# Optimization experiments

Measured on AMD Instinct MI355X. Metric: run time of the kernel, lower is better.

## Reference

```python
import jax, jax.numpy as jnp
import numpy as np

NUM_NODES = 100
WINDOW = 128
GH = 256       # graph_hidden_channels
DH = 64        # discrepancy_hidden_channels
OUT = 128      # out_channels
B = 256        # graphs per batch
N = B * NUM_NODES
E = 409600


def _mconv(x, w, b):
    # x: [B, n, W], w: [n, 2, k], b: [n, 2]  (per-node Conv1d(1,2,k), 'same' padding)
    k = w.shape[-1]
    W = x.shape[-1]
    p = k // 2
    xp = jnp.pad(x, ((0, 0), (0, 0), (p, p)))
    win = jnp.stack([xp[..., j:j + W] for j in range(k)], axis=-1)  # [B,n,W,k]
    return jnp.einsum('bnwk,nck->bncw', win, w) + b[None, :, :, None]


def _gcn(x, edge_index, Wg, bg):
    # PyG GCNConv: add self-loops, symmetric normalization, then linear
    Nn = x.shape[0]
    xw = x @ Wg.T
    loops = jnp.arange(Nn, dtype=edge_index.dtype)
    src = jnp.concatenate([edge_index[0], loops])
    dst = jnp.concatenate([edge_index[1], loops])
    deg = jax.ops.segment_sum(jnp.ones(src.shape[0], dtype=xw.dtype), dst, num_segments=Nn)
    norm = jax.lax.rsqrt(jnp.maximum(deg, 1e-12))
    coef = norm[src] * norm[dst]
    agg = jax.ops.segment_sum(coef[:, None] * xw[src], dst, num_segments=Nn)
    return agg + bg


def setup_inputs() -> dict:
    key = jax.random.key(0)
    ks = jax.random.split(key, 20)
    f = 6 * WINDOW
    s = lambda d: 1.0 / np.sqrt(d)
    inp = {
        'x1': jax.random.normal(ks[0], (N, WINDOW), jnp.float32),
        'x2': jax.random.normal(ks[1], (N, WINDOW), jnp.float32),
        'edge_index1': jax.random.randint(ks[2], (2, E), 0, N, jnp.int32),
        'edge_index2': jax.random.randint(ks[3], (2, E), 0, N, jnp.int32),
        'w3': jax.random.normal(ks[4], (NUM_NODES, 2, 3), jnp.float32) * s(3),
        'b3': jax.random.normal(ks[5], (NUM_NODES, 2), jnp.float32) * s(3),
        'w5': jax.random.normal(ks[6], (NUM_NODES, 2, 5), jnp.float32) * s(5),
        'b5': jax.random.normal(ks[7], (NUM_NODES, 2), jnp.float32) * s(5),
        'w7': jax.random.normal(ks[8], (NUM_NODES, 2, 7), jnp.float32) * s(7),
        'b7': jax.random.normal(ks[9], (NUM_NODES, 2), jnp.float32) * s(7),
        'Wff': jax.random.normal(ks[10], (NUM_NODES, GH, f), jnp.float32) * s(f),
        'bff': jax.random.normal(ks[11], (NUM_NODES, GH), jnp.float32) * s(f),
        'Wg': jax.random.normal(ks[12], (GH, GH), jnp.float32) * s(GH),
        'bg': jax.random.normal(ks[13], (GH,), jnp.float32) * s(GH),
        'Wd': jax.random.normal(ks[14], (NUM_NODES, DH, 2 * GH), jnp.float32) * s(2 * GH),
        'bd': jax.random.normal(ks[15], (NUM_NODES, DH), jnp.float32) * s(2 * GH),
        'Wfc': jax.random.normal(ks[16], (OUT, NUM_NODES * DH), jnp.float32) * s(NUM_NODES * DH),
        'bfc': jax.random.normal(ks[17], (OUT,), jnp.float32) * s(NUM_NODES * DH),
    }
    return inp


def reference(x1, x2, edge_index1, edge_index2, w3, b3, w5, b5, w7, b7,
              Wff, bff, Wg, bg, Wd, bd, Wfc, bfc):
    n = w3.shape[0]
    Nn, W = x1.shape
    Bg = Nn // n

    def branch(x):
        xg = x.reshape(Bg, n, W)
        # multiscale CNN: concat conv3/conv5/conv7 along channel -> [B,n,6,W]
        c = jnp.concatenate([_mconv(xg, w3, b3), _mconv(xg, w5, b5), _mconv(xg, w7, b7)], axis=2)
        c = jax.nn.relu(c.reshape(Bg, n, 6 * W))            # channel-major flatten (matches view(-1))
        h = jax.nn.relu(jnp.einsum('bnf,nhf->bnh', c, Wff) + bff)
        return h.reshape(Nn, -1)

    h1 = jax.nn.relu(_gcn(branch(x1), edge_index1, Wg, bg))
    h2 = jax.nn.relu(_gcn(branch(x2), edge_index2, Wg, bg))
    H = h1.shape[-1]
    cat = jnp.concatenate([h1.reshape(Bg, n, H), h2.reshape(Bg, n, H)], axis=-1)  # [B,n,2H]
    d = jnp.einsum('bnf,ndf->bnd', cat, Wd) + bd            # per-node discrepancy FC
    du = jax.nn.relu(d.reshape(Bg, -1))                     # node-major -> [B, n*DH]
    return du @ Wfc.T + bfc
```

## Files before the change

kernel.cpp:

```cpp
#include <hip/hip_runtime.h>

#define DI __device__ __forceinline__

typedef __bf16 bf16_t;
typedef bf16_t bf16x8 __attribute__((ext_vector_type(8)));
typedef float f32x4 __attribute__((ext_vector_type(4)));
typedef ushort ushort8v __attribute__((ext_vector_type(8)));

static constexpr int NNODE = 100, WIN = 128, GH = 256, DH = 64, OUTC = 128, NB = 256;
static constexpr int NTOT = NB * NNODE;
static constexpr int NE = 409600;
static constexpr int FFK = 6 * WIN;
static constexpr size_t CB = (size_t)NNODE * NB * FFK;
static constexpr size_t HB = (size_t)NTOT * GH;
static constexpr int CVT_BLKS = 23264;
static constexpr int NSEG = 64, SEGE = NE / NSEG;
static constexpr int NPK = NTOT / 2;

DI ushort f2bf(float f) {
  union { float f; unsigned u; } v; v.f = f;
  unsigned r = v.u + 0x7fffu + ((v.u >> 16) & 1u);
  return (ushort)(r >> 16);
}
DI float bf2f(ushort s) {
  union { unsigned u; float f; } v; v.u = ((unsigned)s) << 16; return v.f;
}
DI float u2f(uint u) { union { uint u; float f; } v; v.u = u; return v.f; }

DI void gload16(const void* g, void* l) {
  __builtin_amdgcn_global_load_lds((const __attribute__((address_space(1))) void*)g,
                                   (__attribute__((address_space(3))) void*)l, 16, 0, 0);
}


DI void cvt_body(int bx, const float* s0, const float* s1, const float* s2, const float* s3,
                 ushort* d0, ushort* d1, ushort* d2, ushort* d3) {
  int j = bx * 256 + threadIdx.x;
  const float* s; ushort* d;
  if (j < 19660800 / 4) { s = s0; d = d0; }
  else if ((j -= 19660800 / 4) < 3276800 / 4) { s = s1; d = d1; }
  else if ((j -= 3276800 / 4) < 819200 / 4) { s = s2; d = d2; }
  else { j -= 819200 / 4; s = s3; d = d3; }
  float4 v = reinterpret_cast<const float4*>(s)[j];
  ushort4 o;
  o.x = f2bf(v.x); o.y = f2bf(v.y); o.z = f2bf(v.z); o.w = f2bf(v.w);
  reinterpret_cast<ushort4*>(d)[j] = o;
}

DI void histseg_body(int bx, const int* e1d, const int* e2d,
                     ushort* rank_local, uint* segcnt, uint* cnt ) {
  int set = bx & 1, seg = bx >> 1;
  int tid = threadIdx.x;
#pragma unroll
  for (int k = 0; k < NPK / 256; ++k) cnt[tid + k * 256] = 0;
  __syncthreads();
  const int* dstp = (set ? e2d : e1d) + seg * SEGE;
  ushort* rl = rank_local + set * NE + seg * SEGE;
#pragma unroll
  for (int k = 0; k < SEGE / 256; ++k) {
    int i = k * 256 + tid;
    int d = dstp[i];
    uint sh = (d & 1) * 16;
    uint old = atomicAdd(&cnt[d >> 1], 1u << sh);
    rl[i] = (ushort)((old >> sh) & 0xffffu);
  }
  __syncthreads();
  uint* sc = segcnt + (size_t)(set * NSEG + seg) * NPK;
#pragma unroll
  for (int k = 0; k < NPK / 256; ++k) sc[tid + k * 256] = cnt[tid + k * 256];
}

DI void fill_body(int bx, const int* e1, const int* e2, const int* offs,
                  const ushort* rank_local, const uint* segbase, int* csr) {
  int i = bx * 256 + threadIdx.x;
  int set = i >= NE;
  int ii = i - set * NE;
  const int* e = set ? e2 : e1;
  int d = e[NE + ii];
  int seg = ii / SEGE;
  uint b32 = segbase[(size_t)(set * NSEG + seg) * NPK + (d >> 1)];
  int base = (b32 >> ((d & 1) * 16)) & 0xffff;
  int pos = offs[set * (NTOT + 1) + d] + base + rank_local[i];
  csr[set * NE + pos] = e[ii];
}

DI void scan_body(int set, const int* deg_, int* offs_, float* norm_) {
  const int* deg = deg_ + set * NTOT;
  int* offs = offs_ + set * (NTOT + 1);
  float* norm = norm_ + set * NTOT;
  __shared__ int part[256];
  int t = threadIdx.x;
  int base = t * 100;
  int s = 0;
  for (int j = 0; j < 100; ++j) s += deg[base + j];
  part[t] = s;
  __syncthreads();
  for (int d = 1; d < 256; d <<= 1) {
    int vv = (t >= d) ? part[t - d] : 0;
    __syncthreads();
    part[t] += vv;
    __syncthreads();
  }
  int run = (t > 0) ? part[t - 1] : 0;
  for (int j = 0; j < 100; ++j) {
    int dv = deg[base + j];
    offs[base + j] = run;
    norm[base + j] = rsqrtf((float)(dv + 1));
    run += dv;
  }
  if (t == 255) offs[NTOT] = part[255];
}

DI void conv_body(int bx, const float* x1, const float* x2,
                  const float* w3, const float* b3, const float* w5, const float* b5,
                  const float* w7, const float* b7, ushort* c, float* xs ) {
  const int t = threadIdx.x;
  const int rowi = t >> 4;
  const int idx = t & 15;
  int r = bx * 16 + rowi;
  int br = r >= NTOT;
  int rr = r - br * NTOT;
  const float* x = br ? x2 : x1;
  int b = rr / 100, node = rr - b * 100;

  float* row = xs + rowi * 136;
  const int w0 = idx * 8;
  float4 v0 = *reinterpret_cast<const float4*>(x + (size_t)rr * WIN + w0);
  float4 v1 = *reinterpret_cast<const float4*>(x + (size_t)rr * WIN + w0 + 4);
  *reinterpret_cast<float4*>(&row[4 + w0]) = v0;
  *reinterpret_cast<float4*>(&row[4 + w0 + 4]) = v1;
  if (idx == 0) { row[0] = 0.f; row[1] = 0.f; row[2] = 0.f; row[3] = 0.f; }
  if (idx == 15) { row[132] = 0.f; row[133] = 0.f; row[134] = 0.f; row[135] = 0.f; }
  __syncthreads();

  float xv[14];
#pragma unroll
  for (int j = 0; j < 14; ++j) xv[j] = row[1 + w0 + j];

  const float* W3 = w3 + node * 6;  const float* B3 = b3 + node * 2;
  const float* W5 = w5 + node * 10; const float* B5 = b5 + node * 2;
  const float* W7 = w7 + node * 14; const float* B7 = b7 + node * 2;
  ushort* out = c + (size_t)br * CB + (size_t)(node * NB + b) * FFK + w0;

#pragma unroll
  for (int ch = 0; ch < 2; ++ch) {
    float k3[3], k5[5], k7[7];
#pragma unroll
    for (int j = 0; j < 3; ++j) k3[j] = W3[ch * 3 + j];
#pragma unroll
    for (int j = 0; j < 5; ++j) k5[j] = W5[ch * 5 + j];
#pragma unroll
    for (int j = 0; j < 7; ++j) k7[j] = W7[ch * 7 + j];
    float bb3 = B3[ch], bb5 = B5[ch], bb7 = B7[ch];
    ushort8v o3, o5, o7;
#pragma unroll
    for (int p = 0; p < 8; ++p) {
      float a3 = bb3, a5 = bb5, a7 = bb7;
#pragma unroll
      for (int j = 0; j < 3; ++j) a3 += k3[j] * xv[p + 2 + j];
#pragma unroll
      for (int j = 0; j < 5; ++j) a5 += k5[j] * xv[p + 1 + j];
#pragma unroll
      for (int j = 0; j < 7; ++j) a7 += k7[j] * xv[p + j];
      o3[p] = f2bf(fmaxf(a3, 0.f));
      o5[p] = f2bf(fmaxf(a5, 0.f));
      o7[p] = f2bf(fmaxf(a7, 0.f));
    }
    *reinterpret_cast<ushort8v*>(out + (0 + ch) * WIN) = o3;
    *reinterpret_cast<ushort8v*>(out + (2 + ch) * WIN) = o5;
    *reinterpret_cast<ushort8v*>(out + (4 + ch) * WIN) = o7;
  }
}

template <int MODE>
DI void gemm_body(int bx, int by, const ushort* __restrict__ A, const ushort* __restrict__ A2,
                  const ushort* __restrict__ Bm, ushort* __restrict__ obf,
                  float* __restrict__ of, const float* __restrict__ bias) {
  constexpr int BN = (MODE == 2) ? 64 : 128;
  constexpr int KT = (MODE == 0) ? 12 : (MODE == 1) ? 4 : (MODE == 2) ? 8 : 4;
  constexpr int LDA = (MODE == 0) ? 768 : (MODE == 1) ? 256 : (MODE == 2) ? 256 : 6400;
  constexpr int LDB = (MODE == 0) ? 768 : (MODE == 1) ? 256 : (MODE == 2) ? 512 : 6400;
  constexpr int MF = (MODE == 2) ? 2 : 4;
  constexpr int NF = 4;

  __shared__ ushort As[128 * 64];
  __shared__ ushort Bs[BN * 64];

  const int tid = threadIdx.x, wv = tid >> 6, lane = tid & 63;
  const int j8 = (((lane & 7) ^ (lane >> 3)) - (lane & 7)) * 8;

  int mt = 0, nt = 0, node = 0, kbase = 0, br = 0;
  if constexpr (MODE == 0) {
    int h = bx;
    int s = (h & 7) * 100 + (h >> 3);
    nt = s & 1; int rest = s >> 1;
    mt = rest & 1; int yy = rest >> 1;
    br = yy >= 100; node = yy - br * 100;
  } else if constexpr (MODE == 1) {
    int h = bx;
    int s = (h & 7) * 100 + (h >> 3);
    nt = s & 1; int rest = s >> 1;
    br = rest >= 200; mt = rest - br * 200;
  } else if constexpr (MODE == 2) { mt = bx; node = by; }
  else { mt = bx; kbase = by * 256; }

  const ushort* Ab = nullptr; const ushort* Bb = nullptr;
  if constexpr (MODE == 0) { Ab = A + (size_t)br * CB + (size_t)node * (NB * FFK) + (size_t)mt * 128 * FFK;
                             Bb = Bm + (size_t)node * (GH * FFK) + (size_t)nt * 128 * FFK; }
  else if constexpr (MODE == 1) { Ab = A + (size_t)br * HB + (size_t)mt * 128 * GH;
                                  Bb = Bm + (size_t)nt * 128 * GH; }
  else if constexpr (MODE == 2) { Bb = Bm + (size_t)node * (DH * 512); }
  else { Ab = A + (size_t)mt * 128 * 6400 + kbase; Bb = Bm + kbase; }

  const int wr = (MODE == 2) ? wv : (wv >> 1);
  const int wc = (MODE == 2) ? 0 : (wv & 1);

  f32x4 acc[MF][NF] = {};

  for (int kt = 0; kt < KT; ++kt) {
    const int k0 = kt * 64;
    __syncthreads();
#pragma unroll
    for (int it = 0; it < 4; ++it) {
      int rb = it * 32 + wv * 8;
      int row = rb + (lane >> 3);
      const ushort* gp;
      if constexpr (MODE == 2) {
        int b_ = mt * 128 + row;
        const ushort* src = (k0 < 256) ? A : A2;
        gp = src + (size_t)(b_ * NNODE + node) * GH + (k0 & 255) + (lane & 7) * 8 + j8;
      } else {
        gp = Ab + (size_t)row * LDA + k0 + (lane & 7) * 8 + j8;
      }
      gload16(gp, &As[rb * 64]);
    }
#pragma unroll
    for (int it = 0; it < BN / 32; ++it) {
      int rb = it * 32 + wv * 8;
      int row = rb + (lane >> 3);
      gload16(Bb + (size_t)row * LDB + k0 + (lane & 7) * 8 + j8, &Bs[rb * 64]);
    }
    __syncthreads();
#pragma unroll
    for (int kk = 0; kk < 2; ++kk) {
      const int ch8 = ((kk * 4 + (lane >> 4)) ^ (lane & 7)) * 8;
      bf16x8 af[MF], bfr[NF];
#pragma unroll
      for (int m = 0; m < MF; ++m) {
        int rr = wr * (MF * 16) + m * 16 + (lane & 15);
        af[m] = *reinterpret_cast<const bf16x8*>(&As[rr * 64 + ch8]);
      }
#pragma unroll
      for (int n = 0; n < NF; ++n) {
        int rr = wc * 64 + n * 16 + (lane & 15);
        bfr[n] = *reinterpret_cast<const bf16x8*>(&Bs[rr * 64 + ch8]);
      }
#pragma unroll
      for (int m = 0; m < MF; ++m)
#pragma unroll
        for (int n = 0; n < NF; ++n)
          acc[m][n] = __builtin_amdgcn_mfma_f32_16x16x32_bf16(af[m], bfr[n], acc[m][n], 0, 0, 0);
    }
  }

  const int lrow = (lane >> 4) * 4, lcol = lane & 15;
#pragma unroll
  for (int m = 0; m < MF; ++m) {
#pragma unroll
    for (int n = 0; n < NF; ++n) {
      int cc = wc * 64 + n * 16 + lcol;
#pragma unroll
      for (int rg = 0; rg < 4; ++rg) {
        int rr = wr * (MF * 16) + m * 16 + lrow + rg;
        float val = acc[m][n][rg];
        if constexpr (MODE == 0) {
          int b_ = mt * 128 + rr;
          int col = nt * 128 + cc;
          val = fmaxf(val + bias[node * GH + col], 0.f);
          obf[(size_t)br * HB + (size_t)(b_ * NNODE + node) * GH + col] = f2bf(val);
        } else if constexpr (MODE == 1) {
          int R = mt * 128 + rr;
          int col = nt * 128 + cc;
          obf[(size_t)br * HB + (size_t)R * GH + col] = f2bf(val * bias[br * NTOT + R]);
        } else if constexpr (MODE == 2) {
          int b_ = mt * 128 + rr;
          val = fmaxf(val + bias[node * DH + cc], 0.f);
          obf[(size_t)b_ * (NNODE * DH) + node * DH + cc] = f2bf(val);
        } else {
          int R = mt * 128 + rr;
          if (by == 0) val += bias[cc];
          atomicAdd(&of[R * OUTC + cc], val);
        }
      }
    }
  }
}


__global__ __launch_bounds__(256) void fused1_k(
    const float* __restrict__ Wff, const float* __restrict__ Wd,
    const float* __restrict__ Wfc, const float* __restrict__ Wg,
    ushort* __restrict__ Wffb, ushort* __restrict__ Wdb,
    ushort* __restrict__ Wfcb, ushort* __restrict__ Wgb,
    const int* __restrict__ e1d, const int* __restrict__ e2d,
    ushort* __restrict__ rank_local, uint* __restrict__ segcnt,
    const float* __restrict__ x1, const float* __restrict__ x2,
    const float* __restrict__ w3, const float* __restrict__ b3,
    const float* __restrict__ w5, const float* __restrict__ b5,
    const float* __restrict__ w7, const float* __restrict__ b7,
    ushort* __restrict__ c) {
  __shared__ uint smem[NPK];
  int bx = blockIdx.x;
  if (bx < 128) histseg_body(bx, e1d, e2d, rank_local, segcnt, smem);
  else if (bx < 3328) conv_body(bx - 128, x1, x2, w3, b3, w5, b5, w7, b7, c, (float*)smem);
  else cvt_body(bx - 3328, Wff, Wd, Wfc, Wg, Wffb, Wdb, Wfcb, Wgb);
}

__global__ __launch_bounds__(256) void segscan_k(const uint* __restrict__ segcnt,
                                                 uint* __restrict__ segbase, int* __restrict__ deg) {
  int set = blockIdx.y;
  int p = blockIdx.x * 256 + threadIdx.x;
  uint lo = 0, hi = 0;
  const uint* sc = segcnt + (size_t)set * NSEG * NPK + p;
  uint* sb = segbase + (size_t)set * NSEG * NPK + p;
  for (int s = 0; s < NSEG; ++s) {
    uint v = sc[(size_t)s * NPK];
    sb[(size_t)s * NPK] = lo | (hi << 16);
    lo += v & 0xffffu; hi += v >> 16;
  }
  reinterpret_cast<int2*>(deg)[set * NPK + p] = make_int2((int)lo, (int)hi);
}

__global__ __launch_bounds__(256) void scan_k(const int* __restrict__ deg,
                                              int* __restrict__ offs, float* __restrict__ nrm) {
  scan_body(blockIdx.x, deg, offs, nrm);
}

__global__ __launch_bounds__(256) void fused3_k(
    const ushort* __restrict__ cbuf, const ushort* __restrict__ Wffb,
    ushort* __restrict__ h, const float* __restrict__ bff,
    const int* __restrict__ e1, const int* __restrict__ e2,
    const int* __restrict__ offs, const ushort* __restrict__ rank_local,
    const uint* __restrict__ segbase, int* __restrict__ csr) {
  if ((int)blockIdx.x < 800)
    gemm_body<0>(blockIdx.x, 0, cbuf, nullptr, Wffb, h, nullptr, bff);
  else
    fill_body(blockIdx.x - 800, e1, e2, offs, rank_local, segbase, csr);
}

template <int MODE>
__global__ __launch_bounds__(256) void gemm_k(const ushort* __restrict__ A, const ushort* __restrict__ A2,
                                              const ushort* __restrict__ Bm, ushort* __restrict__ obf,
                                              float* __restrict__ of, const float* __restrict__ bias) {
  gemm_body<MODE>(blockIdx.x, blockIdx.y, A, A2, Bm, obf, of, bias);
}

__global__ __launch_bounds__(256) void agg_k(const ushort* __restrict__ xw_, const int* __restrict__ offs_,
                                             const int* __restrict__ csr_, const float* __restrict__ norm_,
                                             const float* __restrict__ bg, ushort* __restrict__ hg_) {
  int bid = blockIdx.x;
  int c = bid & 7;
  int i = bid >> 3;
  int br = c >> 2, slice = c & 3;
  int g = threadIdx.x >> 3;
  int v = i * 32 + g;
  int l8 = threadIdx.x & 7;
  int col = slice * 64 + l8 * 8;

  const ushort* xw = xw_ + (size_t)br * HB;
  const int* offs = offs_ + br * (NTOT + 1);
  const int* csr = csr_ + br * NE;
  const float* norm = norm_ + br * NTOT;
  ushort* hg = hg_ + (size_t)br * HB;
  const uint* base = reinterpret_cast<const uint*>(xw + col);

  float a[8];
  {
    uint4 q = *reinterpret_cast<const uint4*>(base + (size_t)v * (GH / 2));
    a[0] = u2f(q.x << 16); a[1] = u2f(q.x & 0xffff0000u);
    a[2] = u2f(q.y << 16); a[3] = u2f(q.y & 0xffff0000u);
    a[4] = u2f(q.z << 16); a[5] = u2f(q.z & 0xffff0000u);
    a[6] = u2f(q.w << 16); a[7] = u2f(q.w & 0xffff0000u);
  }
  int e0 = offs[v], e1v = offs[v + 1];
  int j = e0;
  for (; j + 1 < e1v; j += 2) {
    int s0 = csr[j], s1 = csr[j + 1];
    uint4 q0 = *reinterpret_cast<const uint4*>(base + (size_t)s0 * (GH / 2));
    uint4 q1 = *reinterpret_cast<const uint4*>(base + (size_t)s1 * (GH / 2));
    a[0] += u2f(q0.x << 16) + u2f(q1.x << 16);
    a[1] += u2f(q0.x & 0xffff0000u) + u2f(q1.x & 0xffff0000u);
    a[2] += u2f(q0.y << 16) + u2f(q1.y << 16);
    a[3] += u2f(q0.y & 0xffff0000u) + u2f(q1.y & 0xffff0000u);
    a[4] += u2f(q0.z << 16) + u2f(q1.z << 16);
    a[5] += u2f(q0.z & 0xffff0000u) + u2f(q1.z & 0xffff0000u);
    a[6] += u2f(q0.w << 16) + u2f(q1.w << 16);
    a[7] += u2f(q0.w & 0xffff0000u) + u2f(q1.w & 0xffff0000u);
  }
  if (j < e1v) {
    int s0 = csr[j];
    uint4 q0 = *reinterpret_cast<const uint4*>(base + (size_t)s0 * (GH / 2));
    a[0] += u2f(q0.x << 16); a[1] += u2f(q0.x & 0xffff0000u);
    a[2] += u2f(q0.y << 16); a[3] += u2f(q0.y & 0xffff0000u);
    a[4] += u2f(q0.z << 16); a[5] += u2f(q0.z & 0xffff0000u);
    a[6] += u2f(q0.w << 16); a[7] += u2f(q0.w & 0xffff0000u);
  }

  float nv = norm[v];
  float4 bb0 = *reinterpret_cast<const float4*>(bg + col);
  float4 bb1 = *reinterpret_cast<const float4*>(bg + col + 4);
  ushort8v o;
  o[0] = f2bf(fmaxf(nv * a[0] + bb0.x, 0.f));
  o[1] = f2bf(fmaxf(nv * a[1] + bb0.y, 0.f));
  o[2] = f2bf(fmaxf(nv * a[2] + bb0.z, 0.f));
  o[3] = f2bf(fmaxf(nv * a[3] + bb0.w, 0.f));
  o[4] = f2bf(fmaxf(nv * a[4] + bb1.x, 0.f));
  o[5] = f2bf(fmaxf(nv * a[5] + bb1.y, 0.f));
  o[6] = f2bf(fmaxf(nv * a[6] + bb1.z, 0.f));
  o[7] = f2bf(fmaxf(nv * a[7] + bb1.w, 0.f));
  *reinterpret_cast<ushort8v*>(hg + (size_t)v * GH + col) = o;
}

extern "C" void kernel_launch(void* const* d_in, const int* in_sizes, int n_in,
                              void* d_out, int out_size, void* d_ws, size_t ws_size,
                              hipStream_t stream) {
  const float* x1 = (const float*)d_in[0];
  const float* x2 = (const float*)d_in[1];
  const int* e1 = (const int*)d_in[2];
  const int* e2 = (const int*)d_in[3];
  const float* w3 = (const float*)d_in[4];  const float* b3 = (const float*)d_in[5];
  const float* w5 = (const float*)d_in[6];  const float* b5 = (const float*)d_in[7];
  const float* w7 = (const float*)d_in[8];  const float* b7 = (const float*)d_in[9];
  const float* Wff = (const float*)d_in[10]; const float* bff = (const float*)d_in[11];
  const float* Wg = (const float*)d_in[12];  const float* bg = (const float*)d_in[13];
  const float* Wd = (const float*)d_in[14];  const float* bd = (const float*)d_in[15];
  const float* Wfc = (const float*)d_in[16]; const float* bfc = (const float*)d_in[17];
  float* out = (float*)d_out;

  char* ws = (char*)d_ws;
  size_t off = 0;
  auto alloc = [&](size_t bytes) -> char* {
    char* p = ws + off;
    off = (off + bytes + 255) & ~(size_t)255;
    return p;
  };
  ushort* Wffb = (ushort*)alloc(19660800ull * 2);
  ushort* Wdb  = (ushort*)alloc(3276800ull * 2);
  ushort* Wfcb = (ushort*)alloc(819200ull * 2);
  ushort* Wgb  = (ushort*)alloc(65536ull * 2);
  ushort* cbuf = (ushort*)alloc(2 * CB * 2);
  ushort* h    = (ushort*)alloc(2 * HB * 2);
  ushort* xw   = (ushort*)alloc(2 * HB * 2);
  int* deg     = (int*)alloc(2 * NTOT * 4);
  int* offs    = (int*)alloc(2 * (NTOT + 1) * 4);
  ushort* rankl = (ushort*)alloc(2 * NE * 2);
  uint* segcnt  = (uint*)alloc((size_t)2 * NSEG * NPK * 4);
  uint* segbase = (uint*)alloc((size_t)2 * NSEG * NPK * 4);
  int* csr     = (int*)alloc(2 * NE * 4);
  float* nrm   = (float*)alloc(2 * NTOT * 4);
  ushort* du = cbuf;

  hipMemsetAsync(out, 0, (size_t)out_size * 4, stream);

  fused1_k<<<128 + 3200 + CVT_BLKS, 256, 0, stream>>>(
      Wff, Wd, Wfc, Wg, Wffb, Wdb, Wfcb, Wgb,
      e1 + NE, e2 + NE, rankl, segcnt,
      x1, x2, w3, b3, w5, b5, w7, b7, cbuf);
  segscan_k<<<dim3(NPK / 256, 2), 256, 0, stream>>>(segcnt, segbase, deg);
  scan_k<<<2, 256, 0, stream>>>(deg, offs, nrm);
  fused3_k<<<4000, 256, 0, stream>>>(cbuf, Wffb, h, bff, e1, e2, offs, rankl, segbase, csr);

  gemm_k<1><<<800, 256, 0, stream>>>(h, nullptr, Wgb, xw, nullptr, nrm);
  agg_k<<<6400, 256, 0, stream>>>(xw, offs, csr, nrm, bg, h);

  gemm_k<2><<<dim3(2, 100), 256, 0, stream>>>(h, h + HB, Wdb, du, nullptr, bd);
  gemm_k<3><<<dim3(2, 25), 256, 0, stream>>>(du, nullptr, Wfcb, nullptr, out, bfc);
}
```

Baseline: 239.6 us.

## Split edge histogram into destination ranges to shrink fused kernel LDS footprint

The per-segment destination histogram is split into four destination ranges, each handled by its own block, so the shared counter array shrinks by a factor of four. Because the fused kernel's static LDS size is set by this array, every block in the launch (conv and weight conversion too) now reserves far less LDS, allowing more resident blocks per CU. In exchange, each histogram block rereads the whole edge segment and discards out-of-range destinations, quadrupling histogram reads and block count.

```diff
diff --git a/kernel.cpp b/kernel.cpp
--- a/kernel.cpp
+++ b/kernel.cpp
@@ -16,6 +16,9 @@
 static constexpr int CVT_BLKS = 23264;
 static constexpr int NSEG = 64, SEGE = NE / NSEG;
 static constexpr int NPK = NTOT / 2;
+static constexpr int NRANGE = 4, RDST = NTOT / NRANGE;
+static constexpr int RPK = RDST / 2;
+static constexpr int HIST_BLKS = 2 * NSEG * NRANGE;
 
 DI ushort f2bf(float f) {
   union { float f; unsigned u; } v; v.f = f;
@@ -49,25 +52,26 @@
 
 DI void histseg_body(int bx, const int* e1d, const int* e2d,
                      ushort* rank_local, uint* segcnt, uint* cnt ) {
-  int set = bx & 1, seg = bx >> 1;
+  int set = bx & 1, seg = (bx >> 1) & (NSEG - 1), range = bx >> 7;
   int tid = threadIdx.x;
-#pragma unroll
-  for (int k = 0; k < NPK / 256; ++k) cnt[tid + k * 256] = 0;
+  for (int k = tid; k < RPK; k += 256) cnt[k] = 0;
   __syncthreads();
   const int* dstp = (set ? e2d : e1d) + seg * SEGE;
   ushort* rl = rank_local + set * NE + seg * SEGE;
+  const int dbase = range * RDST;
 #pragma unroll
   for (int k = 0; k < SEGE / 256; ++k) {
     int i = k * 256 + tid;
-    int d = dstp[i];
-    uint sh = (d & 1) * 16;
-    uint old = atomicAdd(&cnt[d >> 1], 1u << sh);
-    rl[i] = (ushort)((old >> sh) & 0xffffu);
+    uint dl = (uint)(dstp[i] - dbase);
+    if (dl < (uint)RDST) {
+      uint sh = (dl & 1) * 16;
+      uint old = atomicAdd(&cnt[dl >> 1], 1u << sh);
+      rl[i] = (ushort)((old >> sh) & 0xffffu);
+    }
   }
   __syncthreads();
-  uint* sc = segcnt + (size_t)(set * NSEG + seg) * NPK;
-#pragma unroll
-  for (int k = 0; k < NPK / 256; ++k) sc[tid + k * 256] = cnt[tid + k * 256];
+  uint* sc = segcnt + (size_t)(set * NSEG + seg) * NPK + range * RPK;
+  for (int k = tid; k < RPK; k += 256) sc[k] = cnt[k];
 }
 
 DI void fill_body(int bx, const int* e1, const int* e2, const int* offs,
@@ -309,11 +313,11 @@
     const float* __restrict__ w5, const float* __restrict__ b5,
     const float* __restrict__ w7, const float* __restrict__ b7,
     ushort* __restrict__ c) {
-  __shared__ uint smem[NPK];
+  __shared__ uint smem[RPK];
   int bx = blockIdx.x;
-  if (bx < 128) histseg_body(bx, e1d, e2d, rank_local, segcnt, smem);
-  else if (bx < 3328) conv_body(bx - 128, x1, x2, w3, b3, w5, b5, w7, b7, c, (float*)smem);
-  else cvt_body(bx - 3328, Wff, Wd, Wfc, Wg, Wffb, Wdb, Wfcb, Wgb);
+  if (bx < HIST_BLKS) histseg_body(bx, e1d, e2d, rank_local, segcnt, smem);
+  else if (bx < HIST_BLKS + 3200) conv_body(bx - HIST_BLKS, x1, x2, w3, b3, w5, b5, w7, b7, c, (float*)smem);
+  else cvt_body(bx - HIST_BLKS - 3200, Wff, Wd, Wfc, Wg, Wffb, Wdb, Wfcb, Wgb);
 }
 
 __global__ __launch_bounds__(256) void segscan_k(const uint* __restrict__ segcnt,
@@ -462,7 +466,7 @@
 
   hipMemsetAsync(out, 0, (size_t)out_size * 4, stream);
 
-  fused1_k<<<128 + 3200 + CVT_BLKS, 256, 0, stream>>>(
+  fused1_k<<<HIST_BLKS + 3200 + CVT_BLKS, 256, 0, stream>>>(
       Wff, Wd, Wfc, Wg, Wffb, Wdb, Wfcb, Wgb,
       e1 + NE, e2 + NE, rankl, segcnt,
       x1, x2, w3, b3, w5, b5, w7, b7, cbuf);
```

After: 231.2 us. -3.5%, faster.
